# Kernel tuning notes

Hardware: AMD Instinct MI355X
Metric: run time of the kernel (lower is better)

Reference implementation:

```python
import jax, jax.numpy as jnp
import numpy as np

EPS = 1e-6  # nn.PairwiseDistance default eps, added as x - y + eps before the norm


def setup_inputs() -> dict:
    key = jax.random.key(0)
    k1, k2 = jax.random.split(key)
    class_prototypes = jax.random.normal(k1, (1024, 1024), dtype=jnp.float32)
    query_features = jax.random.normal(k2, (8192, 1024), dtype=jnp.float32)
    return {"class_prototypes": class_prototypes, "query_features": query_features}


def reference(class_prototypes, query_features):
    # dist[i,k] = || q_i - p_k + EPS ||_2  (PairwiseDistance semantics)
    # expand: ||q||^2 + ||p||^2 - 2 q.p + 2*EPS*(sum q - sum p) + D*EPS^2
    D = query_features.shape[1]
    q_sq = jnp.sum(query_features * query_features, axis=1)        # [Q]
    p_sq = jnp.sum(class_prototypes * class_prototypes, axis=1)    # [K]
    cross = query_features @ class_prototypes.T                    # [Q,K]
    lin = 2.0 * EPS * (jnp.sum(query_features, axis=1)[:, None]
                       - jnp.sum(class_prototypes, axis=1)[None, :])
    sq = q_sq[:, None] + p_sq[None, :] - 2.0 * cross + lin + D * EPS * EPS
    dist = jnp.sqrt(jnp.maximum(sq, 0.0))                          # [Q,K]
    post = jnp.exp(-dist)
    post = post / jnp.sum(post, axis=1, keepdims=True)
    c = jnp.max(post, axis=1)
    h = -jnp.sum(post * jnp.log(post), axis=1)
    return (post, c, h)
```

## Files before the change

### kernel.cpp

```cpp
#include <hip/hip_runtime.h>
#include <hip/hip_bf16.h>

#define EPS 1e-6f

typedef float    f32x4  __attribute__((ext_vector_type(4)));
typedef __bf16   bf16x8 __attribute__((ext_vector_type(8)));

static __device__ __forceinline__ unsigned short f2bf(float f) {
    unsigned int x = __float_as_uint(f);
    unsigned int r = (x + 0x7FFFu + ((x >> 16) & 1u)) >> 16;
    return (unsigned short)r;
}

__global__ __launch_bounds__(256) void prep_kernel(const float* __restrict__ src,
                                                   unsigned short* __restrict__ dst,
                                                   float* __restrict__ row_sq,
                                                   float* __restrict__ row_sum) {
    const int row = blockIdx.x;
    const int tid = threadIdx.x;
    const float4 v = reinterpret_cast<const float4*>(src + (size_t)row * 1024)[tid];
    float s  = v.x + v.y + v.z + v.w;
    float ss = v.x * v.x + v.y * v.y + v.z * v.z + v.w * v.w;

    ushort4 b;
    b.x = f2bf(v.x); b.y = f2bf(v.y); b.z = f2bf(v.z); b.w = f2bf(v.w);
    reinterpret_cast<ushort4*>(dst + (size_t)row * 1024)[tid] = b;

    #pragma unroll
    for (int m = 32; m >= 1; m >>= 1) {
        s  += __shfl_xor(s, m, 64);
        ss += __shfl_xor(ss, m, 64);
    }
    __shared__ float red[8];
    const int wave = tid >> 6;
    if ((tid & 63) == 0) { red[wave] = s; red[4 + wave] = ss; }
    __syncthreads();
    if (tid == 0) {
        row_sum[row] = red[0] + red[1] + red[2] + red[3];
        row_sq[row]  = red[4] + red[5] + red[6] + red[7];
    }
}

__global__ __launch_bounds__(256, 2) void gemm_exp_kernel(
    const unsigned short* __restrict__ qb,
    const unsigned short* __restrict__ pb,
    const float* __restrict__ q_sq, const float* __restrict__ q_sum,
    const float* __restrict__ p_sq, const float* __restrict__ p_sum,
    float* __restrict__ e_out,
    float* __restrict__ row_s, float* __restrict__ row_t,
    unsigned int* __restrict__ row_m)
{
    __shared__ unsigned short As[128 * 32];
    __shared__ unsigned short Bs[128 * 32];

    const int tid  = threadIdx.x;
    const int lane = tid & 63;
    const int wave = tid >> 6;
    const int wr = wave >> 1, wc = wave & 1;
    const int l15 = lane & 15;
    const int l4  = lane >> 4;
    const int br = blockIdx.x, bc = blockIdx.y;

    f32x4 acc[4][4];
    #pragma unroll
    for (int m = 0; m < 4; ++m)
        #pragma unroll
        for (int n = 0; n < 4; ++n)
            acc[m][n] = (f32x4)0.0f;

    const size_t qbase = (size_t)(br * 128) * 1024;
    const size_t pbase = (size_t)(bc * 128) * 1024;
    const int c0 = tid, c1 = tid + 256;

    for (int kk = 0; kk < 1024; kk += 32) {
        __syncthreads();
        {
            const unsigned short* gq0 = qb + qbase + (size_t)(c0 >> 2) * 1024 + kk + (c0 & 3) * 8;
            const unsigned short* gq1 = qb + qbase + (size_t)(c1 >> 2) * 1024 + kk + (c1 & 3) * 8;
            const unsigned short* gp0 = pb + pbase + (size_t)(c0 >> 2) * 1024 + kk + (c0 & 3) * 8;
            const unsigned short* gp1 = pb + pbase + (size_t)(c1 >> 2) * 1024 + kk + (c1 & 3) * 8;
            __builtin_amdgcn_global_load_lds((const __attribute__((address_space(1))) void*)gq0,
                                             (__attribute__((address_space(3))) void*)(&As[c0 * 8]), 16, 0, 0);
            __builtin_amdgcn_global_load_lds((const __attribute__((address_space(1))) void*)gq1,
                                             (__attribute__((address_space(3))) void*)(&As[c1 * 8]), 16, 0, 0);
            __builtin_amdgcn_global_load_lds((const __attribute__((address_space(1))) void*)gp0,
                                             (__attribute__((address_space(3))) void*)(&Bs[c0 * 8]), 16, 0, 0);
            __builtin_amdgcn_global_load_lds((const __attribute__((address_space(1))) void*)gp1,
                                             (__attribute__((address_space(3))) void*)(&Bs[c1 * 8]), 16, 0, 0);
        }
        __syncthreads();

        bf16x8 a[4], b[4];
        #pragma unroll
        for (int m = 0; m < 4; ++m)
            a[m] = *reinterpret_cast<const bf16x8*>(&As[(wr * 64 + m * 16 + l15) * 32 + l4 * 8]);
        #pragma unroll
        for (int n = 0; n < 4; ++n)
            b[n] = *reinterpret_cast<const bf16x8*>(&Bs[(wc * 64 + n * 16 + l15) * 32 + l4 * 8]);
        #pragma unroll
        for (int m = 0; m < 4; ++m)
            #pragma unroll
            for (int n = 0; n < 4; ++n)
                acc[m][n] = __builtin_amdgcn_mfma_f32_16x16x32_bf16(a[m], b[n], acc[m][n], 0, 0, 0);
    }

    const int row0 = br * 128 + wr * 64;
    const int col0 = bc * 128 + wc * 64;

    float ps[4], pm[4];
    #pragma unroll
    for (int n = 0; n < 4; ++n) {
        const int c = col0 + n * 16 + l15;
        ps[n] = p_sq[c];
        pm[n] = p_sum[c];
    }
    const float dee = 1024.0f * EPS * EPS;

    #pragma unroll
    for (int m = 0; m < 4; ++m) {
        #pragma unroll
        for (int r = 0; r < 4; ++r) {
            const int row = row0 + m * 16 + l4 * 4 + r;
            const float qs = q_sq[row], qm = q_sum[row];
            float se = 0.0f, te = 0.0f, mx = 0.0f;
            #pragma unroll
            for (int n = 0; n < 4; ++n) {
                const float cross = acc[m][n][r];
                const float sq = qs + ps[n] - 2.0f * cross + 2.0f * EPS * (qm - pm[n]) + dee;
                const float dist = sqrtf(fmaxf(sq, 0.0f));
                const float e = __expf(-dist);
                e_out[(size_t)row * 1024 + (col0 + n * 16 + l15)] = e;
                se += e;
                te += e * dist;
                mx = fmaxf(mx, e);
            }
            #pragma unroll
            for (int msk = 8; msk >= 1; msk >>= 1) {
                se += __shfl_xor(se, msk, 64);
                te += __shfl_xor(te, msk, 64);
                mx = fmaxf(mx, __shfl_xor(mx, msk, 64));
            }
            if (l15 == 0) {
                atomicAdd(&row_s[row], se);
                atomicAdd(&row_t[row], te);
                atomicMax(&row_m[row], __float_as_uint(mx));
            }
        }
    }
}

__global__ __launch_bounds__(256) void finalize_kernel(const float* __restrict__ row_s,
                                                       const float* __restrict__ row_t,
                                                       const unsigned int* __restrict__ row_m,
                                                       float* __restrict__ c_out,
                                                       float* __restrict__ h_out,
                                                       float* __restrict__ inv_s) {
    const int i = blockIdx.x * 256 + threadIdx.x;
    const float s = row_s[i];
    const float inv = 1.0f / s;
    inv_s[i] = inv;
    c_out[i] = __uint_as_float(row_m[i]) * inv;
    h_out[i] = logf(s) + row_t[i] * inv;
}

__global__ __launch_bounds__(256) void normalize_kernel(float* __restrict__ post,
                                                        const float* __restrict__ inv_s) {
    const int idx = blockIdx.x * 256 + threadIdx.x;
    const int row = idx >> 8;
    float4* p = reinterpret_cast<float4*>(post);
    float4 v = p[idx];
    const float inv = inv_s[row];
    v.x *= inv; v.y *= inv; v.z *= inv; v.w *= inv;
    p[idx] = v;
}

extern "C" void kernel_launch(void* const* d_in, const int* in_sizes, int n_in,
                              void* d_out, int out_size, void* d_ws, size_t ws_size,
                              hipStream_t stream) {
    const float* protos = (const float*)d_in[0];
    const float* querys = (const float*)d_in[1];

    float* out   = (float*)d_out;
    float* post  = out;
    float* c_out = out + (size_t)8192 * 1024;
    float* h_out = c_out + 8192;

    char* ws = (char*)d_ws;
    unsigned short* qb = (unsigned short*)ws;  ws += (size_t)8192 * 1024 * 2;
    unsigned short* pb = (unsigned short*)ws;  ws += (size_t)1024 * 1024 * 2;
    float* q_sq  = (float*)ws;  ws += 8192 * 4;
    float* q_sum = (float*)ws;  ws += 8192 * 4;
    float* p_sq  = (float*)ws;  ws += 1024 * 4;
    float* p_sum = (float*)ws;  ws += 1024 * 4;
    float* row_s = (float*)ws;  ws += 8192 * 4;
    float* row_t = (float*)ws;  ws += 8192 * 4;
    unsigned int* row_m = (unsigned int*)ws;  ws += 8192 * 4;
    float* inv_s = (float*)ws;  ws += 8192 * 4;

    (void)hipMemsetAsync(row_s, 0, 3 * 8192 * sizeof(float), stream);

    prep_kernel<<<8192, 256, 0, stream>>>(querys, qb, q_sq, q_sum);
    prep_kernel<<<1024, 256, 0, stream>>>(protos, pb, p_sq, p_sum);
    gemm_exp_kernel<<<dim3(64, 8), 256, 0, stream>>>(qb, pb, q_sq, q_sum, p_sq, p_sum,
                                                     post, row_s, row_t, row_m);
    finalize_kernel<<<32, 256, 0, stream>>>(row_s, row_t, row_m, c_out, h_out, inv_s);
    normalize_kernel<<<8192, 256, 0, stream>>>(post, inv_s);
}
```

Baseline: 139.8 us.

## Fuse GEMM, softmax-normalize and stats into one full-row kernel

```diff
diff --git a/kernel.cpp b/kernel.cpp
--- a/kernel.cpp
+++ b/kernel.cpp
@@ -3,8 +3,8 @@
 
 #define EPS 1e-6f
 
-typedef float    f32x4  __attribute__((ext_vector_type(4)));
-typedef __bf16   bf16x8 __attribute__((ext_vector_type(8)));
+typedef float  f32x4  __attribute__((ext_vector_type(4)));
+typedef __bf16 bf16x8 __attribute__((ext_vector_type(8)));
 
 static __device__ __forceinline__ unsigned short f2bf(float f) {
     unsigned int x = __float_as_uint(f);
@@ -12,19 +12,31 @@
     return (unsigned short)r;
 }
 
-__global__ __launch_bounds__(256) void prep_kernel(const float* __restrict__ src,
-                                                   unsigned short* __restrict__ dst,
-                                                   float* __restrict__ row_sq,
-                                                   float* __restrict__ row_sum) {
-    const int row = blockIdx.x;
+__global__ __launch_bounds__(256) void prep_kernel(
+    const float* __restrict__ protos, const float* __restrict__ querys,
+    unsigned short* __restrict__ pb, unsigned short* __restrict__ qb,
+    float* __restrict__ p_sq, float* __restrict__ p_sum,
+    float* __restrict__ q_sq, float* __restrict__ q_sum)
+{
+    const int b   = blockIdx.x;
     const int tid = threadIdx.x;
-    const float4 v = reinterpret_cast<const float4*>(src + (size_t)row * 1024)[tid];
+    const float* src; unsigned short* dst; float* rsq; float* rsum;
+    if (b < 1024) {
+        src = protos + (size_t)b * 1024; dst = pb + (size_t)b * 1024;
+        rsq = p_sq + b; rsum = p_sum + b;
+    } else {
+        const int r = b - 1024;
+        src = querys + (size_t)r * 1024; dst = qb + (size_t)r * 1024;
+        rsq = q_sq + r; rsum = q_sum + r;
+    }
+
+    const float4 v = reinterpret_cast<const float4*>(src)[tid];
     float s  = v.x + v.y + v.z + v.w;
     float ss = v.x * v.x + v.y * v.y + v.z * v.z + v.w * v.w;
 
-    ushort4 b;
-    b.x = f2bf(v.x); b.y = f2bf(v.y); b.z = f2bf(v.z); b.w = f2bf(v.w);
-    reinterpret_cast<ushort4*>(dst + (size_t)row * 1024)[tid] = b;
+    ushort4 o;
+    o.x = f2bf(v.x); o.y = f2bf(v.y); o.z = f2bf(v.z); o.w = f2bf(v.w);
+    reinterpret_cast<ushort4*>(dst)[tid] = o;
 
     #pragma unroll
     for (int m = 32; m >= 1; m >>= 1) {
@@ -36,100 +48,106 @@
     if ((tid & 63) == 0) { red[wave] = s; red[4 + wave] = ss; }
     __syncthreads();
     if (tid == 0) {
-        row_sum[row] = red[0] + red[1] + red[2] + red[3];
-        row_sq[row]  = red[4] + red[5] + red[6] + red[7];
-    }
-}
-
-__global__ __launch_bounds__(256, 2) void gemm_exp_kernel(
+        *rsum = red[0] + red[1] + red[2] + red[3];
+        *rsq  = red[4] + red[5] + red[6] + red[7];
+    }
+}
+
+__global__ __launch_bounds__(512, 2) void fused_kernel(
     const unsigned short* __restrict__ qb,
     const unsigned short* __restrict__ pb,
     const float* __restrict__ q_sq, const float* __restrict__ q_sum,
     const float* __restrict__ p_sq, const float* __restrict__ p_sum,
-    float* __restrict__ e_out,
-    float* __restrict__ row_s, float* __restrict__ row_t,
-    unsigned int* __restrict__ row_m)
+    float* __restrict__ post, float* __restrict__ c_out, float* __restrict__ h_out)
 {
-    __shared__ unsigned short As[128 * 32];
-    __shared__ unsigned short Bs[128 * 32];
+    __shared__ float se_l[8][32];
+    __shared__ float te_l[8][32];
+    __shared__ float mx_l[8][32];
+    __shared__ float qs_l[32], qm_l[32], inv_l[32];
 
     const int tid  = threadIdx.x;
+    const int w    = tid >> 6;
     const int lane = tid & 63;
-    const int wave = tid >> 6;
-    const int wr = wave >> 1, wc = wave & 1;
-    const int l15 = lane & 15;
-    const int l4  = lane >> 4;
-    const int br = blockIdx.x, bc = blockIdx.y;
-
-    f32x4 acc[4][4];
-    #pragma unroll
-    for (int m = 0; m < 4; ++m)
-        #pragma unroll
-        for (int n = 0; n < 4; ++n)
-            acc[m][n] = (f32x4)0.0f;
-
-    const size_t qbase = (size_t)(br * 128) * 1024;
-    const size_t pbase = (size_t)(bc * 128) * 1024;
-    const int c0 = tid, c1 = tid + 256;
-
-    for (int kk = 0; kk < 1024; kk += 32) {
-        __syncthreads();
-        {
-            const unsigned short* gq0 = qb + qbase + (size_t)(c0 >> 2) * 1024 + kk + (c0 & 3) * 8;
-            const unsigned short* gq1 = qb + qbase + (size_t)(c1 >> 2) * 1024 + kk + (c1 & 3) * 8;
-            const unsigned short* gp0 = pb + pbase + (size_t)(c0 >> 2) * 1024 + kk + (c0 & 3) * 8;
-            const unsigned short* gp1 = pb + pbase + (size_t)(c1 >> 2) * 1024 + kk + (c1 & 3) * 8;
-            __builtin_amdgcn_global_load_lds((const __attribute__((address_space(1))) void*)gq0,
-                                             (__attribute__((address_space(3))) void*)(&As[c0 * 8]), 16, 0, 0);
-            __builtin_amdgcn_global_load_lds((const __attribute__((address_space(1))) void*)gq1,
-                                             (__attribute__((address_space(3))) void*)(&As[c1 * 8]), 16, 0, 0);
-            __builtin_amdgcn_global_load_lds((const __attribute__((address_space(1))) void*)gp0,
-                                             (__attribute__((address_space(3))) void*)(&Bs[c0 * 8]), 16, 0, 0);
-            __builtin_amdgcn_global_load_lds((const __attribute__((address_space(1))) void*)gp1,
-                                             (__attribute__((address_space(3))) void*)(&Bs[c1 * 8]), 16, 0, 0);
-        }
-        __syncthreads();
-
-        bf16x8 a[4], b[4];
-        #pragma unroll
-        for (int m = 0; m < 4; ++m)
-            a[m] = *reinterpret_cast<const bf16x8*>(&As[(wr * 64 + m * 16 + l15) * 32 + l4 * 8]);
-        #pragma unroll
-        for (int n = 0; n < 4; ++n)
-            b[n] = *reinterpret_cast<const bf16x8*>(&Bs[(wc * 64 + n * 16 + l15) * 32 + l4 * 8]);
-        #pragma unroll
-        for (int m = 0; m < 4; ++m)
-            #pragma unroll
-            for (int n = 0; n < 4; ++n)
-                acc[m][n] = __builtin_amdgcn_mfma_f32_16x16x32_bf16(a[m], b[n], acc[m][n], 0, 0, 0);
-    }
-
-    const int row0 = br * 128 + wr * 64;
-    const int col0 = bc * 128 + wc * 64;
-
-    float ps[4], pm[4];
-    #pragma unroll
-    for (int n = 0; n < 4; ++n) {
+    const int l15  = lane & 15;
+    const int l4   = lane >> 4;
+    const int row0 = blockIdx.x * 32;
+    const int col0 = w * 128;
+
+    if (tid < 32) { qs_l[tid] = q_sq[row0 + tid]; qm_l[tid] = q_sum[row0 + tid]; }
+    __syncthreads();
+
+    float ps[8], pm[8];
+    #pragma unroll
+    for (int n = 0; n < 8; ++n) {
         const int c = col0 + n * 16 + l15;
         ps[n] = p_sq[c];
         pm[n] = p_sum[c];
     }
+
+    const unsigned short* ap[2];
+    const unsigned short* bp[8];
+    #pragma unroll
+    for (int m = 0; m < 2; ++m)
+        ap[m] = qb + (size_t)(row0 + m * 16 + l15) * 1024 + l4 * 8;
+    #pragma unroll
+    for (int n = 0; n < 8; ++n)
+        bp[n] = pb + (size_t)(col0 + n * 16 + l15) * 1024 + l4 * 8;
+
+    f32x4 acc[2][8];
+    #pragma unroll
+    for (int m = 0; m < 2; ++m)
+        #pragma unroll
+        for (int n = 0; n < 8; ++n)
+            acc[m][n] = (f32x4)0.0f;
+
+    bf16x8 a0[2], b0[8], a1[2], b1[8];
+
+#define LOADF(A, B, KK) do {                                                    \
+    _Pragma("unroll")                                                           \
+    for (int m = 0; m < 2; ++m) A[m] = *reinterpret_cast<const bf16x8*>(ap[m] + (KK)); \
+    _Pragma("unroll")                                                           \
+    for (int n = 0; n < 8; ++n) B[n] = *reinterpret_cast<const bf16x8*>(bp[n] + (KK)); \
+} while (0)
+
+#define MM(A, B) do {                                                           \
+    _Pragma("unroll")                                                           \
+    for (int m = 0; m < 2; ++m)                                                 \
+        _Pragma("unroll")                                                       \
+        for (int n = 0; n < 8; ++n)                                             \
+            acc[m][n] = __builtin_amdgcn_mfma_f32_16x16x32_bf16(A[m], B[n], acc[m][n], 0, 0, 0); \
+} while (0)
+
+    LOADF(a0, b0, 0);
+    #pragma unroll 1
+    for (int kk = 0; kk < 960; kk += 64) {
+        LOADF(a1, b1, kk + 32);
+        MM(a0, b0);
+        LOADF(a0, b0, kk + 64);
+        MM(a1, b1);
+    }
+    LOADF(a1, b1, 992);
+    MM(a0, b0);
+    MM(a1, b1);
+
+#undef LOADF
+#undef MM
+
     const float dee = 1024.0f * EPS * EPS;
 
     #pragma unroll
-    for (int m = 0; m < 4; ++m) {
+    for (int m = 0; m < 2; ++m) {
         #pragma unroll
         for (int r = 0; r < 4; ++r) {
-            const int row = row0 + m * 16 + l4 * 4 + r;
-            const float qs = q_sq[row], qm = q_sum[row];
+            const int lr = m * 16 + l4 * 4 + r;
+            const float qs = qs_l[lr], qm = qm_l[lr];
             float se = 0.0f, te = 0.0f, mx = 0.0f;
             #pragma unroll
-            for (int n = 0; n < 4; ++n) {
+            for (int n = 0; n < 8; ++n) {
                 const float cross = acc[m][n][r];
                 const float sq = qs + ps[n] - 2.0f * cross + 2.0f * EPS * (qm - pm[n]) + dee;
                 const float dist = sqrtf(fmaxf(sq, 0.0f));
                 const float e = __expf(-dist);
-                e_out[(size_t)row * 1024 + (col0 + n * 16 + l15)] = e;
+                acc[m][n][r] = e;
                 se += e;
                 te += e * dist;
                 mx = fmaxf(mx, e);
@@ -141,37 +159,41 @@
                 mx = fmaxf(mx, __shfl_xor(mx, msk, 64));
             }
             if (l15 == 0) {
-                atomicAdd(&row_s[row], se);
-                atomicAdd(&row_t[row], te);
-                atomicMax(&row_m[row], __float_as_uint(mx));
+                se_l[w][lr] = se;
+                te_l[w][lr] = te;
+                mx_l[w][lr] = mx;
             }
         }
     }
-}
-
-__global__ __launch_bounds__(256) void finalize_kernel(const float* __restrict__ row_s,
-                                                       const float* __restrict__ row_t,
-                                                       const unsigned int* __restrict__ row_m,
-                                                       float* __restrict__ c_out,
-                                                       float* __restrict__ h_out,
-                                                       float* __restrict__ inv_s) {
-    const int i = blockIdx.x * 256 + threadIdx.x;
-    const float s = row_s[i];
-    const float inv = 1.0f / s;
-    inv_s[i] = inv;
-    c_out[i] = __uint_as_float(row_m[i]) * inv;
-    h_out[i] = logf(s) + row_t[i] * inv;
-}
-
-__global__ __launch_bounds__(256) void normalize_kernel(float* __restrict__ post,
-                                                        const float* __restrict__ inv_s) {
-    const int idx = blockIdx.x * 256 + threadIdx.x;
-    const int row = idx >> 8;
-    float4* p = reinterpret_cast<float4*>(post);
-    float4 v = p[idx];
-    const float inv = inv_s[row];
-    v.x *= inv; v.y *= inv; v.z *= inv; v.w *= inv;
-    p[idx] = v;
+    __syncthreads();
+
+    if (tid < 32) {
+        float s = 0.0f, t = 0.0f, mx = 0.0f;
+        #pragma unroll
+        for (int ww = 0; ww < 8; ++ww) {
+            s += se_l[ww][tid];
+            t += te_l[ww][tid];
+            mx = fmaxf(mx, mx_l[ww][tid]);
+        }
+        const float inv = 1.0f / s;
+        inv_l[tid] = inv;
+        c_out[row0 + tid] = mx * inv;
+        h_out[row0 + tid] = logf(s) + t * inv;
+    }
+    __syncthreads();
+
+    #pragma unroll
+    for (int m = 0; m < 2; ++m) {
+        #pragma unroll
+        for (int r = 0; r < 4; ++r) {
+            const int lr = m * 16 + l4 * 4 + r;
+            const float inv = inv_l[lr];
+            #pragma unroll
+            for (int n = 0; n < 8; ++n) {
+                post[(size_t)(row0 + lr) * 1024 + col0 + n * 16 + l15] = acc[m][n][r] * inv;
+            }
+        }
+    }
 }
 
 extern "C" void kernel_launch(void* const* d_in, const int* in_sizes, int n_in,
@@ -192,17 +214,8 @@
     float* q_sum = (float*)ws;  ws += 8192 * 4;
     float* p_sq  = (float*)ws;  ws += 1024 * 4;
     float* p_sum = (float*)ws;  ws += 1024 * 4;
-    float* row_s = (float*)ws;  ws += 8192 * 4;
-    float* row_t = (float*)ws;  ws += 8192 * 4;
-    unsigned int* row_m = (unsigned int*)ws;  ws += 8192 * 4;
-    float* inv_s = (float*)ws;  ws += 8192 * 4;
-
-    (void)hipMemsetAsync(row_s, 0, 3 * 8192 * sizeof(float), stream);
-
-    prep_kernel<<<8192, 256, 0, stream>>>(querys, qb, q_sq, q_sum);
-    prep_kernel<<<1024, 256, 0, stream>>>(protos, pb, p_sq, p_sum);
-    gemm_exp_kernel<<<dim3(64, 8), 256, 0, stream>>>(qb, pb, q_sq, q_sum, p_sq, p_sum,
-                                                     post, row_s, row_t, row_m);
-    finalize_kernel<<<32, 256, 0, stream>>>(row_s, row_t, row_m, c_out, h_out, inv_s);
-    normalize_kernel<<<8192, 256, 0, stream>>>(post, inv_s);
-}
+
+    prep_kernel<<<9216, 256, 0, stream>>>(protos, querys, pb, qb, p_sq, p_sum, q_sq, q_sum);
+    fused_kernel<<<256, 512, 0, stream>>>(qb, pb, q_sq, q_sum, p_sq, p_sum,
+                                          post, c_out, h_out);
+}
```

Measured after the change: 169.9 us. 21.5% more time.

## Store unnormalized exp in bf16 and fuse normalize with finalize

Applied to the files above, without the earlier changes.

```diff
diff --git a/kernel.cpp b/kernel.cpp
--- a/kernel.cpp
+++ b/kernel.cpp
@@ -3,28 +3,43 @@
 
 #define EPS 1e-6f
 
-typedef float    f32x4  __attribute__((ext_vector_type(4)));
-typedef __bf16   bf16x8 __attribute__((ext_vector_type(8)));
+typedef float  f32x4  __attribute__((ext_vector_type(4)));
+typedef __bf16 bf16x8 __attribute__((ext_vector_type(8)));
 
 static __device__ __forceinline__ unsigned short f2bf(float f) {
     unsigned int x = __float_as_uint(f);
     unsigned int r = (x + 0x7FFFu + ((x >> 16) & 1u)) >> 16;
     return (unsigned short)r;
 }
-
-__global__ __launch_bounds__(256) void prep_kernel(const float* __restrict__ src,
-                                                   unsigned short* __restrict__ dst,
-                                                   float* __restrict__ row_sq,
-                                                   float* __restrict__ row_sum) {
-    const int row = blockIdx.x;
+static __device__ __forceinline__ float bf2f(unsigned short u) {
+    return __uint_as_float((unsigned int)u << 16);
+}
+
+__global__ __launch_bounds__(256) void prep_kernel(
+    const float* __restrict__ protos, const float* __restrict__ querys,
+    unsigned short* __restrict__ pb, unsigned short* __restrict__ qb,
+    float* __restrict__ p_sq, float* __restrict__ p_sum,
+    float* __restrict__ q_sq, float* __restrict__ q_sum)
+{
+    const int b   = blockIdx.x;
     const int tid = threadIdx.x;
-    const float4 v = reinterpret_cast<const float4*>(src + (size_t)row * 1024)[tid];
+    const float* src; unsigned short* dst; float* rsq; float* rsum;
+    if (b < 1024) {
+        src = protos + (size_t)b * 1024; dst = pb + (size_t)b * 1024;
+        rsq = p_sq + b; rsum = p_sum + b;
+    } else {
+        const int r = b - 1024;
+        src = querys + (size_t)r * 1024; dst = qb + (size_t)r * 1024;
+        rsq = q_sq + r; rsum = q_sum + r;
+    }
+
+    const float4 v = reinterpret_cast<const float4*>(src)[tid];
     float s  = v.x + v.y + v.z + v.w;
     float ss = v.x * v.x + v.y * v.y + v.z * v.z + v.w * v.w;
 
-    ushort4 b;
-    b.x = f2bf(v.x); b.y = f2bf(v.y); b.z = f2bf(v.z); b.w = f2bf(v.w);
-    reinterpret_cast<ushort4*>(dst + (size_t)row * 1024)[tid] = b;
+    ushort4 o;
+    o.x = f2bf(v.x); o.y = f2bf(v.y); o.z = f2bf(v.z); o.w = f2bf(v.w);
+    reinterpret_cast<ushort4*>(dst)[tid] = o;
 
     #pragma unroll
     for (int m = 32; m >= 1; m >>= 1) {
@@ -36,8 +51,8 @@
     if ((tid & 63) == 0) { red[wave] = s; red[4 + wave] = ss; }
     __syncthreads();
     if (tid == 0) {
-        row_sum[row] = red[0] + red[1] + red[2] + red[3];
-        row_sq[row]  = red[4] + red[5] + red[6] + red[7];
+        *rsum = red[0] + red[1] + red[2] + red[3];
+        *rsq  = red[4] + red[5] + red[6] + red[7];
     }
 }
 
@@ -46,7 +61,7 @@
     const unsigned short* __restrict__ pb,
     const float* __restrict__ q_sq, const float* __restrict__ q_sum,
     const float* __restrict__ p_sq, const float* __restrict__ p_sum,
-    float* __restrict__ e_out,
+    unsigned short* __restrict__ e_out,
     float* __restrict__ row_s, float* __restrict__ row_t,
     unsigned int* __restrict__ row_m)
 {
@@ -129,7 +144,7 @@
                 const float sq = qs + ps[n] - 2.0f * cross + 2.0f * EPS * (qm - pm[n]) + dee;
                 const float dist = sqrtf(fmaxf(sq, 0.0f));
                 const float e = __expf(-dist);
-                e_out[(size_t)row * 1024 + (col0 + n * 16 + l15)] = e;
+                e_out[(size_t)row * 1024 + (col0 + n * 16 + l15)] = f2bf(e);
                 se += e;
                 te += e * dist;
                 mx = fmaxf(mx, e);
@@ -149,29 +164,27 @@
     }
 }
 
-__global__ __launch_bounds__(256) void finalize_kernel(const float* __restrict__ row_s,
-                                                       const float* __restrict__ row_t,
-                                                       const unsigned int* __restrict__ row_m,
-                                                       float* __restrict__ c_out,
-                                                       float* __restrict__ h_out,
-                                                       float* __restrict__ inv_s) {
-    const int i = blockIdx.x * 256 + threadIdx.x;
-    const float s = row_s[i];
+__global__ __launch_bounds__(256) void normfin_kernel(
+    const unsigned short* __restrict__ e16,
+    const float* __restrict__ row_s, const float* __restrict__ row_t,
+    const unsigned int* __restrict__ row_m,
+    float* __restrict__ post, float* __restrict__ c_out, float* __restrict__ h_out)
+{
+    const int row = blockIdx.x;
+    const int tid = threadIdx.x;
+    const float s   = row_s[row];
     const float inv = 1.0f / s;
-    inv_s[i] = inv;
-    c_out[i] = __uint_as_float(row_m[i]) * inv;
-    h_out[i] = logf(s) + row_t[i] * inv;
-}
-
-__global__ __launch_bounds__(256) void normalize_kernel(float* __restrict__ post,
-                                                        const float* __restrict__ inv_s) {
-    const int idx = blockIdx.x * 256 + threadIdx.x;
-    const int row = idx >> 8;
-    float4* p = reinterpret_cast<float4*>(post);
-    float4 v = p[idx];
-    const float inv = inv_s[row];
-    v.x *= inv; v.y *= inv; v.z *= inv; v.w *= inv;
-    p[idx] = v;
+    if (tid == 0) {
+        c_out[row] = __uint_as_float(row_m[row]) * inv;
+        h_out[row] = logf(s) + row_t[row] * inv;
+    }
+    const ushort4 ev = reinterpret_cast<const ushort4*>(e16 + (size_t)row * 1024)[tid];
+    float4 o;
+    o.x = bf2f(ev.x) * inv;
+    o.y = bf2f(ev.y) * inv;
+    o.z = bf2f(ev.z) * inv;
+    o.w = bf2f(ev.w) * inv;
+    reinterpret_cast<float4*>(post + (size_t)row * 1024)[tid] = o;
 }
 
 extern "C" void kernel_launch(void* const* d_in, const int* in_sizes, int n_in,
@@ -186,8 +199,9 @@
     float* h_out = c_out + 8192;
 
     char* ws = (char*)d_ws;
-    unsigned short* qb = (unsigned short*)ws;  ws += (size_t)8192 * 1024 * 2;
-    unsigned short* pb = (unsigned short*)ws;  ws += (size_t)1024 * 1024 * 2;
+    unsigned short* qb  = (unsigned short*)ws;  ws += (size_t)8192 * 1024 * 2;
+    unsigned short* pb  = (unsigned short*)ws;  ws += (size_t)1024 * 1024 * 2;
+    unsigned short* e16 = (unsigned short*)ws;  ws += (size_t)8192 * 1024 * 2;
     float* q_sq  = (float*)ws;  ws += 8192 * 4;
     float* q_sum = (float*)ws;  ws += 8192 * 4;
     float* p_sq  = (float*)ws;  ws += 1024 * 4;
@@ -195,14 +209,11 @@
     float* row_s = (float*)ws;  ws += 8192 * 4;
     float* row_t = (float*)ws;  ws += 8192 * 4;
     unsigned int* row_m = (unsigned int*)ws;  ws += 8192 * 4;
-    float* inv_s = (float*)ws;  ws += 8192 * 4;
 
     (void)hipMemsetAsync(row_s, 0, 3 * 8192 * sizeof(float), stream);
 
-    prep_kernel<<<8192, 256, 0, stream>>>(querys, qb, q_sq, q_sum);
-    prep_kernel<<<1024, 256, 0, stream>>>(protos, pb, p_sq, p_sum);
+    prep_kernel<<<9216, 256, 0, stream>>>(protos, querys, pb, qb, p_sq, p_sum, q_sq, q_sum);
     gemm_exp_kernel<<<dim3(64, 8), 256, 0, stream>>>(qb, pb, q_sq, q_sum, p_sq, p_sum,
-                                                     post, row_s, row_t, row_m);
-    finalize_kernel<<<32, 256, 0, stream>>>(row_s, row_t, row_m, c_out, h_out, inv_s);
-    normalize_kernel<<<8192, 256, 0, stream>>>(post, inv_s);
-}
+                                                     e16, row_s, row_t, row_m);
+    normfin_kernel<<<8192, 256, 0, stream>>>(e16, row_s, row_t, row_m, post, c_out, h_out);
+}
```

Result: faster. 132.4 us (-5.3%).
